# Optimization experiments

Measured on AMD Instinct MI355X. Metric: run time of the kernel, lower is better.

The kernel has to match this reference:

```python
import jax, jax.numpy as jnp
import numpy as np

DIM = 1024
HEADS = 8
DIM_HEAD = 64
INNER = HEADS * DIM_HEAD
NQ = 4096
NKV = 4096
SCALE = DIM_HEAD ** (-0.5)
NEG = -1.0e9


def setup_inputs() -> dict:
    key = jax.random.key(0)
    ks = jax.random.split(key, 7)
    s = DIM ** (-0.5)
    x = jax.random.normal(ks[0], (NQ, DIM), dtype=jnp.float32)
    y = jax.random.normal(ks[1], (NKV, DIM), dtype=jnp.float32)
    # binary mask: 1 => blocked (gets -1e9 added), 0 => attend
    mask = jax.random.randint(ks[2], (NQ, NKV), 0, 2).astype(jnp.float32)
    Wq = jax.random.normal(ks[3], (DIM, INNER), dtype=jnp.float32) * s
    Wk = jax.random.normal(ks[4], (DIM, INNER), dtype=jnp.float32) * s
    Wv = jax.random.normal(ks[5], (DIM, INNER), dtype=jnp.float32) * s
    Wo = jax.random.normal(ks[6], (INNER, DIM), dtype=jnp.float32) * (INNER ** -0.5)
    return {"x": x, "y": y, "mask": mask, "Wq": Wq, "Wk": Wk, "Wv": Wv, "Wo": Wo}


def reference(x, y, mask, Wq, Wk, Wv, Wo):
    # q scaled before projection split, as in the torch module
    q = (x @ Wq) * SCALE                      # [NQ, INNER]
    k = y @ Wk                                # [NKV, INNER]
    v = y @ Wv                                # [NKV, INNER]
    qh = q.reshape(NQ, HEADS, DIM_HEAD)
    kh = k.reshape(NKV, HEADS, DIM_HEAD)
    vh = v.reshape(NKV, HEADS, DIM_HEAD)
    # per-head QK^T + additive mask (mask shared across heads), then softmax
    scores = jnp.einsum('nhd,mhd->hnm', qh, kh) + mask * NEG  # [H, NQ, NKV]
    attn = jax.nn.softmax(scores, axis=-1)
    outh = jnp.einsum('hnm,mhd->nhd', attn, vh)               # [NQ, H, D]
    out = outh.reshape(NQ, INNER) @ Wo                        # [NQ, DIM]
    return out
```

## Files before the change

### kernel.cpp

```cpp
#include <hip/hip_runtime.h>

#define DIMM   1024
#define INNER  512
#define HEADS  8
#define DH     64
#define NQ     4096
#define NKV    4096
#define NSPLIT 4
#define KVCHUNK (NKV / NSPLIT)
#define QBLK   32
#define MWORDS (NKV / 32)
#define LOG2E  (1.44269504089f)
#define SM_C   (-17.3123404907f)

typedef __attribute__((ext_vector_type(8))) short s16x8;
typedef __attribute__((ext_vector_type(4))) short s16x4;
typedef __attribute__((ext_vector_type(4))) float f32x4;
typedef __attribute__((ext_vector_type(4))) unsigned int u32x4;
typedef short s16x2a __attribute__((ext_vector_type(2), may_alias));
typedef s16x8 s16x8a __attribute__((may_alias));

__device__ __forceinline__ short f2b(float x) {
    unsigned int u = __float_as_uint(x);
    unsigned int r = (u + 0x7fffu + ((u >> 16) & 1u)) >> 16;
    return (short)r;
}

__device__ __forceinline__ float fast_exp2(float x) {
#if __has_builtin(__builtin_amdgcn_exp2f)
    return __builtin_amdgcn_exp2f(x);
#else
    return exp2f(x);
#endif
}

__global__ __launch_bounds__(256) void conv_w(const float* __restrict__ Wq,
                                              const float* __restrict__ Wk,
                                              const float* __restrict__ Wv,
                                              const float* __restrict__ Wo,
                                              short* __restrict__ Wcat,
                                              short* __restrict__ Wot) {
    int idx = blockIdx.x * 256 + threadIdx.x;
    int which = idx >> 19;
    int e = idx & 524287;
    if (which == 3) { int k = e >> 10, n = e & 1023; Wot[(size_t)n * INNER + k] = f2b(Wo[e]); }
    else {
        const float* W = (which == 0) ? Wq : (which == 1) ? Wk : Wv;
        float sc = (which == 0) ? 0.125f : 1.0f;
        int k = e >> 9, n = e & 511;
        Wcat[(size_t)(which * 512 + n) * DIMM + k] = f2b(W[e] * sc);
    }
}

__global__ __launch_bounds__(256) void conv_mask(const float* __restrict__ mask,
                                                 unsigned int* __restrict__ Mb) {
    int wg = blockIdx.x * 4 + (threadIdx.x >> 6);
    int l = threadIdx.x & 63;
    for (int itr = 0; itr < 32; ++itr) {
        size_t i = (size_t)wg * 32 + itr;
        int q = (int)(i >> 6), c = (int)(i & 63);
        float v = mask[(size_t)q * NKV + c * 64 + l];
        unsigned long long b = __ballot(v != 0.0f);
        if ((l & 31) == 0) Mb[(size_t)q * MWORDS + c * 2 + (l >> 5)] = (unsigned int)(b >> l);
    }
}

__global__ __launch_bounds__(256) void gemm_qkv(const float* __restrict__ x,
                                                const float* __restrict__ y,
                                                const short* __restrict__ Wcat,
                                                short* __restrict__ Qb,
                                                short* __restrict__ Kb,
                                                short* __restrict__ Vt) {
    __shared__ __align__(16) short Ash[64 * 40];
    __shared__ __align__(16) short Bsh[128 * 40];
    const int t = threadIdx.x, w = t >> 6, l = t & 63, l15 = l & 15, q4 = l >> 4;
    const int m0 = blockIdx.x * 64;
    const int by = blockIdx.y;
    const int n0 = by * 128;
    const float* A = (by < 4) ? x : y;
    const int wm = (w >> 1) * 32, wn = (w & 1) * 64;
    f32x4 acc[2][4] = {};

    const int arow = t >> 2, aseg = t & 3;

    for (int ks = 0; ks < DIMM; ks += 32) {
        __syncthreads();
        {
            const f32x4* pa = (const f32x4*)&A[(size_t)(m0 + arow) * DIMM + ks + aseg * 8];
            f32x4 a0 = pa[0], a1 = pa[1];
            s16x8 ab;
#pragma unroll
            for (int j = 0; j < 4; ++j) { ab[j] = f2b(a0[j]); ab[4 + j] = f2b(a1[j]); }
            *(s16x8*)&Ash[arow * 40 + aseg * 8] = ab;
        }
#pragma unroll
        for (int j = 0; j < 2; ++j) {
            int c = t + j * 256;
            int row = c >> 2, seg = c & 3;
            s16x8 vb = *(const s16x8*)&Wcat[(size_t)(n0 + row) * DIMM + ks + seg * 8];
            *(s16x8*)&Bsh[row * 40 + seg * 8] = vb;
        }
        __syncthreads();
        s16x8 af[2], bf[4];
#pragma unroll
        for (int i = 0; i < 2; ++i) af[i] = *(const s16x8*)&Ash[(wm + i * 16 + l15) * 40 + q4 * 8];
#pragma unroll
        for (int i = 0; i < 4; ++i) bf[i] = *(const s16x8*)&Bsh[(wn + i * 16 + l15) * 40 + q4 * 8];
#pragma unroll
        for (int mi = 0; mi < 2; ++mi)
#pragma unroll
            for (int ni = 0; ni < 4; ++ni)
                acc[mi][ni] = __builtin_amdgcn_mfma_f32_16x16x32_bf16(af[mi], bf[ni], acc[mi][ni], 0, 0, 0);
    }

#pragma unroll
    for (int mi = 0; mi < 2; ++mi)
#pragma unroll
        for (int ni = 0; ni < 4; ++ni)
#pragma unroll
            for (int r = 0; r < 4; ++r) {
                int row = m0 + wm + mi * 16 + q4 * 4 + r;
                int n = n0 + wn + ni * 16 + l15;
                short b = f2b(acc[mi][ni][r]);
                if (n < 512)       Qb[(size_t)row * INNER + n] = b;
                else if (n < 1024) Kb[(size_t)row * INNER + (n - 512)] = b;
                else               Vt[(size_t)(n - 1024) * NKV + row] = b;
            }
}

__global__ __launch_bounds__(256) void attn_fused(const short* __restrict__ Qb,
                                                  const short* __restrict__ Kb,
                                                  const short* __restrict__ Vt,
                                                  const unsigned int* __restrict__ Mb,
                                                  float* __restrict__ Op,
                                                  float* __restrict__ lpart) {
    __shared__ __align__(16) unsigned int Msh[32 * 32];
    __shared__ __align__(16) short Psh[4 * 32 * 40];
    const int t = threadIdx.x, w = t >> 6, l = t & 63, l15 = l & 15, q4 = l >> 4;
    const int b = blockIdx.x;
    const int sh8 = b & 7;
    const int split = sh8 >> 1;
    const int h = (sh8 & 1) * 4 + w;
    const int q0 = (b >> 3) * QBLK;
    const int kv_base = split * KVCHUNK;
    short* Pw = Psh + w * (32 * 40);

    {
        int it = t & 31, r8 = t >> 5;
#pragma unroll
        for (int jj = 0; jj < 4; ++jj) {
            int row = r8 + jj * 8;
            Msh[it * 32 + row] = Mb[(size_t)(q0 + row) * MWORDS + split * 32 + it];
        }
    }

    s16x8 qf[2][2];
#pragma unroll
    for (int mi = 0; mi < 2; ++mi)
#pragma unroll
        for (int kb = 0; kb < 2; ++kb)
            qf[mi][kb] = *(const s16x8*)&Qb[(size_t)(q0 + mi * 16 + l15) * INNER + h * DH + kb * 32 + q4 * 8];

    __syncthreads();

    f32x4 accO[2][4] = {};
    float lsum[2][4] = {};

#pragma unroll 2
    for (int it = 0; it < KVCHUNK / 32; ++it) {
        const int kv0 = kv_base + it * 32;
        s16x8 kf[2][2];
#pragma unroll
        for (int ni = 0; ni < 2; ++ni)
#pragma unroll
            for (int kb = 0; kb < 2; ++kb)
                kf[ni][kb] = *(const s16x8*)&Kb[(size_t)(kv0 + 2 * l15 + ni) * INNER + h * DH + kb * 32 + q4 * 8];
        s16x8 vf[4];
#pragma unroll
        for (int ni = 0; ni < 4; ++ni)
            vf[ni] = *(const s16x8*)&Vt[(size_t)(h * DH + ni * 16 + l15) * NKV + kv0 + q4 * 8];

        f32x4 sf[2][2] = {};
#pragma unroll
        for (int mi = 0; mi < 2; ++mi)
#pragma unroll
            for (int ni = 0; ni < 2; ++ni) {
                sf[mi][ni] = __builtin_amdgcn_mfma_f32_16x16x32_bf16(qf[mi][0], kf[ni][0], sf[mi][ni], 0, 0, 0);
                sf[mi][ni] = __builtin_amdgcn_mfma_f32_16x16x32_bf16(qf[mi][1], kf[ni][1], sf[mi][ni], 0, 0, 0);
            }

#pragma unroll
        for (int mi = 0; mi < 2; ++mi) {
            u32x4 w4 = *(const u32x4*)&Msh[it * 32 + mi * 16 + q4 * 4];
#pragma unroll
            for (int r = 0; r < 4; ++r) {
                unsigned int shb = w4[r] >> (2 * l15);
                float e0 = fast_exp2(fmaf(sf[mi][0][r], LOG2E, SM_C));
                float e1 = fast_exp2(fmaf(sf[mi][1][r], LOG2E, SM_C));
                float p0 = (shb & 1u) ? 0.0f : e0;
                float p1 = (shb & 2u) ? 0.0f : e1;
                lsum[mi][r] += p0 + p1;
                unsigned int pk;
                asm("v_cvt_pk_bf16_f32 %0, %1, %2" : "=v"(pk) : "v"(p0), "v"(p1));
                *(s16x2a*)&Pw[(mi * 16 + q4 * 4 + r) * 40 + 2 * l15] = __builtin_bit_cast(s16x2a, pk);
            }
        }

        s16x8 pf[2];
#pragma unroll
        for (int mi = 0; mi < 2; ++mi)
            pf[mi] = (s16x8)(*(const s16x8a*)&Pw[(mi * 16 + l15) * 40 + q4 * 8]);
#pragma unroll
        for (int mi = 0; mi < 2; ++mi)
#pragma unroll
            for (int ni = 0; ni < 4; ++ni)
                accO[mi][ni] = __builtin_amdgcn_mfma_f32_16x16x32_bf16(pf[mi], vf[ni], accO[mi][ni], 0, 0, 0);
    }

#pragma unroll
    for (int mi = 0; mi < 2; ++mi)
#pragma unroll
        for (int ni = 0; ni < 4; ++ni)
#pragma unroll
            for (int r = 0; r < 4; ++r) {
                int q = q0 + mi * 16 + q4 * 4 + r;
                Op[((size_t)split * NQ + q) * INNER + h * DH + ni * 16 + l15] = accO[mi][ni][r];
            }
#pragma unroll
    for (int mi = 0; mi < 2; ++mi)
#pragma unroll
        for (int r = 0; r < 4; ++r) {
            float s = lsum[mi][r];
            s += __shfl_xor(s, 1);
            s += __shfl_xor(s, 2);
            s += __shfl_xor(s, 4);
            s += __shfl_xor(s, 8);
            lsum[mi][r] = s;
        }
    if (l15 == 0) {
#pragma unroll
        for (int mi = 0; mi < 2; ++mi)
#pragma unroll
            for (int r = 0; r < 4; ++r) {
                int q = q0 + mi * 16 + q4 * 4 + r;
                lpart[((size_t)split * NQ + q) * HEADS + h] = lsum[mi][r];
            }
    }
}

__global__ __launch_bounds__(256) void merge_kernel(const float* __restrict__ Op,
                                                    const float* __restrict__ lpart,
                                                    short* __restrict__ AO) {
    int idx = blockIdx.x * 256 + threadIdx.x;
    int q = idx >> 6, dc = idx & 63, h = dc >> 3;
    float L = 0.f;
#pragma unroll
    for (int s = 0; s < NSPLIT; ++s) L += lpart[((size_t)s * NQ + q) * HEADS + h];
    f32x4 a0 = {}, a1 = {};
#pragma unroll
    for (int s = 0; s < NSPLIT; ++s) {
        const f32x4* p = (const f32x4*)&Op[((size_t)s * NQ + q) * INNER + dc * 8];
        a0 += p[0];
        a1 += p[1];
    }
    float inv = 1.0f / L;
    s16x8 o;
#pragma unroll
    for (int j = 0; j < 4; ++j) o[j] = f2b(a0[j] * inv);
#pragma unroll
    for (int j = 0; j < 4; ++j) o[4 + j] = f2b(a1[j] * inv);
    *(s16x8*)&AO[(size_t)q * INNER + dc * 8] = o;
}

__global__ __launch_bounds__(256) void gemm_out(const short* __restrict__ A,
                                                const short* __restrict__ Bt,
                                                float* __restrict__ C) {
    __shared__ __align__(16) short Ash[64 * 40];
    __shared__ __align__(16) short Bsh[128 * 40];
    const int t = threadIdx.x, w = t >> 6, l = t & 63, l15 = l & 15, q4 = l >> 4;
    const int m0 = blockIdx.x * 64, n0 = blockIdx.y * 128;
    const int wm = (w >> 1) * 32, wn = (w & 1) * 64;
    f32x4 acc[2][4] = {};
    const int arow = t >> 2, aseg = t & 3;

    for (int ks = 0; ks < INNER; ks += 32) {
        __syncthreads();
        {
            s16x8 va = *(const s16x8*)&A[(size_t)(m0 + arow) * INNER + ks + aseg * 8];
            *(s16x8*)&Ash[arow * 40 + aseg * 8] = va;
        }
#pragma unroll
        for (int j = 0; j < 2; ++j) {
            int c = t + j * 256;
            int row = c >> 2, seg = c & 3;
            s16x8 vb = *(const s16x8*)&Bt[(size_t)(n0 + row) * INNER + ks + seg * 8];
            *(s16x8*)&Bsh[row * 40 + seg * 8] = vb;
        }
        __syncthreads();
        s16x8 af[2], bf[4];
#pragma unroll
        for (int i = 0; i < 2; ++i) af[i] = *(const s16x8*)&Ash[(wm + i * 16 + l15) * 40 + q4 * 8];
#pragma unroll
        for (int i = 0; i < 4; ++i) bf[i] = *(const s16x8*)&Bsh[(wn + i * 16 + l15) * 40 + q4 * 8];
#pragma unroll
        for (int mi = 0; mi < 2; ++mi)
#pragma unroll
            for (int ni = 0; ni < 4; ++ni)
                acc[mi][ni] = __builtin_amdgcn_mfma_f32_16x16x32_bf16(af[mi], bf[ni], acc[mi][ni], 0, 0, 0);
    }

#pragma unroll
    for (int mi = 0; mi < 2; ++mi)
#pragma unroll
        for (int ni = 0; ni < 4; ++ni)
#pragma unroll
            for (int r = 0; r < 4; ++r) {
                int row = m0 + wm + mi * 16 + q4 * 4 + r;
                int col = n0 + wn + ni * 16 + l15;
                C[(size_t)row * DIMM + col] = acc[mi][ni][r];
            }
}

extern "C" void kernel_launch(void* const* d_in, const int* in_sizes, int n_in,
                              void* d_out, int out_size, void* d_ws, size_t ws_size,
                              hipStream_t stream) {
    const float* x    = (const float*)d_in[0];
    const float* y    = (const float*)d_in[1];
    const float* mask = (const float*)d_in[2];
    const float* Wq   = (const float*)d_in[3];
    const float* Wk   = (const float*)d_in[4];
    const float* Wv   = (const float*)d_in[5];
    const float* Wo   = (const float*)d_in[6];
    float* out = (float*)d_out;

    char* ws = (char*)d_ws;
    float* Op    = (float*)(ws + (size_t)0);
    short* Qb    = (short*)(ws + ((size_t)32 << 20));
    short* Kb    = (short*)(ws + ((size_t)36 << 20));
    short* Vtb   = (short*)(ws + ((size_t)40 << 20));
    short* AO    = (short*)(ws + ((size_t)44 << 20));
    unsigned int* Mb = (unsigned int*)(ws + ((size_t)48 << 20));
    float* lpart = (float*)(ws + ((size_t)50 << 20));
    short* Wcat  = (short*)(ws + ((size_t)51 << 20));
    short* Wot   = (short*)(ws + ((size_t)54 << 20));

    hipLaunchKernelGGL(conv_w,    dim3(8192), dim3(256), 0, stream, Wq, Wk, Wv, Wo, Wcat, Wot);
    hipLaunchKernelGGL(conv_mask, dim3(2048), dim3(256), 0, stream, mask, Mb);
    hipLaunchKernelGGL(gemm_qkv,  dim3(64, 12), dim3(256), 0, stream, x, y, Wcat, Qb, Kb, Vtb);
    hipLaunchKernelGGL(attn_fused, dim3((NQ / QBLK) * NSPLIT * 2), dim3(256), 0, stream,
                       Qb, Kb, Vtb, Mb, Op, lpart);
    hipLaunchKernelGGL(merge_kernel, dim3(1024), dim3(256), 0, stream, Op, lpart, AO);
    hipLaunchKernelGGL(gemm_out,  dim3(64, 8), dim3(256), 0, stream, AO, Wot, out);
}
```

Before: 332.6 us.

## Double attention KV splits and store split partials in bf16

```diff
diff --git a/kernel.cpp b/kernel.cpp
--- a/kernel.cpp
+++ b/kernel.cpp
@@ -6,10 +6,11 @@
 #define DH     64
 #define NQ     4096
 #define NKV    4096
-#define NSPLIT 4
+#define NSPLIT 8
 #define KVCHUNK (NKV / NSPLIT)
 #define QBLK   32
 #define MWORDS (NKV / 32)
+#define SWORDS (KVCHUNK / 32)
 #define LOG2E  (1.44269504089f)
 #define SM_C   (-17.3123404907f)
 
@@ -24,6 +25,11 @@
     unsigned int u = __float_as_uint(x);
     unsigned int r = (u + 0x7fffu + ((u >> 16) & 1u)) >> 16;
     return (short)r;
+}
+
+__device__ __forceinline__ float b2f(short b) {
+    unsigned int u = ((unsigned int)(unsigned short)b) << 16;
+    return __uint_as_float(u);
 }
 
 __device__ __forceinline__ float fast_exp2(float x) {
@@ -132,25 +138,25 @@
                                                   const short* __restrict__ Kb,
                                                   const short* __restrict__ Vt,
                                                   const unsigned int* __restrict__ Mb,
-                                                  float* __restrict__ Op,
+                                                  short* __restrict__ Op,
                                                   float* __restrict__ lpart) {
-    __shared__ __align__(16) unsigned int Msh[32 * 32];
+    __shared__ __align__(16) unsigned int Msh[SWORDS * 32];
     __shared__ __align__(16) short Psh[4 * 32 * 40];
     const int t = threadIdx.x, w = t >> 6, l = t & 63, l15 = l & 15, q4 = l >> 4;
     const int b = blockIdx.x;
-    const int sh8 = b & 7;
-    const int split = sh8 >> 1;
-    const int h = (sh8 & 1) * 4 + w;
-    const int q0 = (b >> 3) * QBLK;
+    const int combo = b & 15;
+    const int split = combo >> 1;
+    const int h = (combo & 1) * 4 + w;
+    const int q0 = (b >> 4) * QBLK;
     const int kv_base = split * KVCHUNK;
     short* Pw = Psh + w * (32 * 40);
 
     {
-        int it = t & 31, r8 = t >> 5;
-#pragma unroll
-        for (int jj = 0; jj < 4; ++jj) {
-            int row = r8 + jj * 8;
-            Msh[it * 32 + row] = Mb[(size_t)(q0 + row) * MWORDS + split * 32 + it];
+        int it = t & 15, r16 = t >> 4;
+#pragma unroll
+        for (int jj = 0; jj < 2; ++jj) {
+            int row = r16 + jj * 16;
+            Msh[it * 32 + row] = Mb[(size_t)(q0 + row) * MWORDS + split * SWORDS + it];
         }
     }
 
@@ -166,7 +172,6 @@
     f32x4 accO[2][4] = {};
     float lsum[2][4] = {};
 
-#pragma unroll 2
     for (int it = 0; it < KVCHUNK / 32; ++it) {
         const int kv0 = kv_base + it * 32;
         s16x8 kf[2][2];
@@ -224,7 +229,7 @@
 #pragma unroll
             for (int r = 0; r < 4; ++r) {
                 int q = q0 + mi * 16 + q4 * 4 + r;
-                Op[((size_t)split * NQ + q) * INNER + h * DH + ni * 16 + l15] = accO[mi][ni][r];
+                Op[((size_t)split * NQ + q) * INNER + h * DH + ni * 16 + l15] = f2b(accO[mi][ni][r]);
             }
 #pragma unroll
     for (int mi = 0; mi < 2; ++mi)
@@ -248,7 +253,7 @@
     }
 }
 
-__global__ __launch_bounds__(256) void merge_kernel(const float* __restrict__ Op,
+__global__ __launch_bounds__(256) void merge_kernel(const short* __restrict__ Op,
                                                     const float* __restrict__ lpart,
                                                     short* __restrict__ AO) {
     int idx = blockIdx.x * 256 + threadIdx.x;
@@ -256,19 +261,17 @@
     float L = 0.f;
 #pragma unroll
     for (int s = 0; s < NSPLIT; ++s) L += lpart[((size_t)s * NQ + q) * HEADS + h];
-    f32x4 a0 = {}, a1 = {};
+    float a[8] = {};
 #pragma unroll
     for (int s = 0; s < NSPLIT; ++s) {
-        const f32x4* p = (const f32x4*)&Op[((size_t)s * NQ + q) * INNER + dc * 8];
-        a0 += p[0];
-        a1 += p[1];
+        s16x8 v = *(const s16x8*)&Op[((size_t)s * NQ + q) * INNER + dc * 8];
+#pragma unroll
+        for (int j = 0; j < 8; ++j) a[j] += b2f(v[j]);
     }
     float inv = 1.0f / L;
     s16x8 o;
 #pragma unroll
-    for (int j = 0; j < 4; ++j) o[j] = f2b(a0[j] * inv);
-#pragma unroll
-    for (int j = 0; j < 4; ++j) o[4 + j] = f2b(a1[j] * inv);
+    for (int j = 0; j < 8; ++j) o[j] = f2b(a[j] * inv);
     *(s16x8*)&AO[(size_t)q * INNER + dc * 8] = o;
 }
 
@@ -334,7 +337,7 @@
     float* out = (float*)d_out;
 
     char* ws = (char*)d_ws;
-    float* Op    = (float*)(ws + (size_t)0);
+    short* Op    = (short*)(ws + (size_t)0);
     short* Qb    = (short*)(ws + ((size_t)32 << 20));
     short* Kb    = (short*)(ws + ((size_t)36 << 20));
     short* Vtb   = (short*)(ws + ((size_t)40 << 20));
```

Result: no change. 336.7 us (+1.2%).
